# Kernel optimization log

Hardware: AMD Instinct MI355X
Metric: run time of the kernel (lower is better)

The kernel has to match this reference:

```python
import math
import jax, jax.numpy as jnp
import numpy as np

D_MODEL = 1024
NHEAD = 16
DK = D_MODEL // NHEAD
FACTOR = 5
B, L = 4, 8192
U = max(1, min(FACTOR * math.ceil(math.log(L + 1)), L))  # 50


def setup_inputs() -> dict:
    key = jax.random.key(0)
    ks = jax.random.split(key, 10)
    s = 1.0 / math.sqrt(D_MODEL)
    inp = {
        "x": jax.random.normal(ks[0], (B, L, D_MODEL), dtype=jnp.float32),
        "Wq": jax.random.normal(ks[1], (D_MODEL, D_MODEL), dtype=jnp.float32) * s,
        "bq": jnp.zeros((D_MODEL,), dtype=jnp.float32),
        "Wk": jax.random.normal(ks[2], (D_MODEL, D_MODEL), dtype=jnp.float32) * s,
        "bk": jnp.zeros((D_MODEL,), dtype=jnp.float32),
        "Wv": jax.random.normal(ks[3], (D_MODEL, D_MODEL), dtype=jnp.float32) * s,
        "bv": jnp.zeros((D_MODEL,), dtype=jnp.float32),
        "Wo": jax.random.normal(ks[4], (D_MODEL, D_MODEL), dtype=jnp.float32) * s,
        "bo": jnp.zeros((D_MODEL,), dtype=jnp.float32),
        # randperm(L)[:U] sample of key positions (constant, like torch.randperm)
        "idx_k": jax.random.permutation(ks[5], L)[:U].astype(jnp.int32),
    }
    return inp


def reference(x, Wq, bq, Wk, bk, Wv, bv, Wo, bo, idx_k):
    Bv, Lv, _ = x.shape
    H, dk = NHEAD, DK
    u = idx_k.shape[0]
    scale = 1.0 / math.sqrt(dk)

    # projections -> [B, H, L, dk]
    Q = (x @ Wq.T + bq).reshape(Bv, Lv, H, dk).transpose(0, 2, 1, 3)
    K = (x @ Wk.T + bk).reshape(Bv, Lv, H, dk).transpose(0, 2, 1, 3)
    V = (x @ Wv.T + bv).reshape(Bv, Lv, H, dk).transpose(0, 2, 1, 3)

    # sampled scores against u random keys: [B, H, L, u]
    K_samp = K[:, :, idx_k, :]
    scores = jnp.einsum("bhld,bhud->bhlu", Q, K_samp) * scale
    M = scores.max(-1) - scores.mean(-1)                 # [B, H, L]
    _, top_idx = jax.lax.top_k(M, u)                      # [B, H, u]

    # gather selected queries and attend against ALL keys
    Q_top = jnp.take_along_axis(Q, top_idx[..., None], axis=2)   # [B, H, u, dk]
    attn = jax.nn.softmax(jnp.einsum("bhud,bhld->bhul", Q_top, K) * scale, axis=-1)
    ctx_top = jnp.einsum("bhul,bhld->bhud", attn, V)              # [B, H, u, dk]

    # mean(V) fallback, scatter selected contexts back
    ctx = jnp.broadcast_to(V.mean(axis=2, keepdims=True), (Bv, H, Lv, dk))
    bidx = jnp.arange(Bv)[:, None, None]
    hidx = jnp.arange(H)[None, :, None]
    ctx = ctx.at[bidx, hidx, top_idx].set(ctx_top)

    ctx = ctx.transpose(0, 2, 1, 3).reshape(Bv, Lv, H * dk)
    return ctx @ Wo.T + bo
```

## Files before the change

kernel.cpp:

```cpp
#include <hip/hip_runtime.h>
#include <hip/hip_bf16.h>

#define B_ 4
#define L_ 8192
#define D_ 1024
#define H_ 16
#define SCALE 0.125f
#define NC 8
#define QPAD 64
#define RS 72

typedef __attribute__((ext_vector_type(8))) short bf16x8;
typedef __attribute__((ext_vector_type(4))) float f32x4;

__device__ __forceinline__ float blo(unsigned v) { return __uint_as_float(v << 16); }
__device__ __forceinline__ float bhi(unsigned v) { return __uint_as_float(v & 0xffff0000u); }

__device__ __forceinline__ void gl2lds16(const void* g, void* s) {
    __builtin_amdgcn_global_load_lds(
        (const __attribute__((address_space(1))) unsigned int*)g,
        (__attribute__((address_space(3))) unsigned int*)s, 16, 0, 0);
}

__device__ __forceinline__ unsigned short bfbits(float a) {
    __hip_bfloat16 h = __float2bfloat16(a);
    return *(unsigned short*)&h;
}
__device__ __forceinline__ float bf2f(unsigned short u) {
    return __uint_as_float(((unsigned)u) << 16);
}

__global__ __launch_bounds__(256) void split3_kernel(const float* __restrict__ in,
        unsigned short* __restrict__ ph, unsigned short* __restrict__ pm,
        unsigned short* __restrict__ pl, int n4) {
    int i = blockIdx.x * 256 + threadIdx.x;
    if (i >= n4) return;
    float4 v = ((const float4*)in)[i];
    float c[4] = {v.x, v.y, v.z, v.w};
    unsigned short h[4], m[4], l[4];
    #pragma unroll
    for (int j = 0; j < 4; ++j) {
        float a = c[j];
        unsigned short hb = bfbits(a);
        float rh = a - bf2f(hb);
        unsigned short mb = bfbits(rh);
        float rm = rh - bf2f(mb);
        h[j] = hb; m[j] = mb; l[j] = bfbits(rm);
    }
    ((ushort4*)ph)[i] = *(ushort4*)h;
    ((ushort4*)pm)[i] = *(ushort4*)m;
    ((ushort4*)pl)[i] = *(ushort4*)l;
}

__global__ __launch_bounds__(256) void split2_kernel(const float* __restrict__ in,
        unsigned short* __restrict__ ph, unsigned short* __restrict__ pm, int n4) {
    int i = blockIdx.x * 256 + threadIdx.x;
    if (i >= n4) return;
    float4 v = ((const float4*)in)[i];
    float c[4] = {v.x, v.y, v.z, v.w};
    unsigned short h[4], m[4];
    #pragma unroll
    for (int j = 0; j < 4; ++j) {
        float a = c[j];
        unsigned short hb = bfbits(a);
        float rh = a - bf2f(hb);
        h[j] = hb; m[j] = bfbits(rh);
    }
    ((ushort4*)ph)[i] = *(ushort4*)h;
    ((ushort4*)pm)[i] = *(ushort4*)m;
}

__global__ __launch_bounds__(256) void xmean_kernel(const float* __restrict__ x,
                                                    float* __restrict__ xmean) {
    int c = blockIdx.x;
    int j = blockIdx.y * 256 + threadIdx.x;
    int b = blockIdx.z;
    const float* xp = x + ((size_t)b * L_ + (size_t)c * 256) * D_ + j;
    float s = 0.f;
    for (int l = 0; l < 256; ++l) s += xp[(size_t)l * D_];
    atomicAdd(&xmean[b * D_ + j], s * (1.0f / L_));
}

__global__ __launch_bounds__(256) void vecmat_kernel(const float* __restrict__ in,
                                                     const float* __restrict__ W,
                                                     const float* __restrict__ bias,
                                                     float* __restrict__ out) {
    __shared__ float vs[D_];
    int b = blockIdx.y;
    int j = blockIdx.x * 256 + threadIdx.x;
    for (int t = threadIdx.x; t < D_; t += 256) vs[t] = in[b * D_ + t];
    __syncthreads();
    const float* wr = W + (size_t)j * D_;
    float acc = 0.f;
    #pragma unroll 4
    for (int k = 0; k < D_; k += 4) {
        float4 w4 = *(const float4*)(wr + k);
        acc += vs[k] * w4.x + vs[k + 1] * w4.y + vs[k + 2] * w4.z + vs[k + 3] * w4.w;
    }
    out[b * D_ + j] = acc + bias[j];
}

__global__ __launch_bounds__(256) void ksamp_kernel(const float* __restrict__ x,
                                                    const float* __restrict__ Wk,
                                                    const float* __restrict__ bk,
                                                    const int* __restrict__ idx_k,
                                                    float* __restrict__ Ksamp, int U) {
    __shared__ float vs[D_];
    int u = blockIdx.x, b = blockIdx.y;
    int row = idx_k[u];
    const float* xp = x + ((size_t)b * L_ + row) * D_;
    for (int t = threadIdx.x; t < D_; t += 256) vs[t] = xp[t];
    __syncthreads();
    #pragma unroll
    for (int r = 0; r < 4; ++r) {
        int j = r * 256 + threadIdx.x;
        const float* wr = Wk + (size_t)j * D_;
        float acc = 0.f;
        #pragma unroll 4
        for (int k = 0; k < D_; k += 4) {
            float4 w4 = *(const float4*)(wr + k);
            acc += vs[k] * w4.x + vs[k + 1] * w4.y + vs[k + 2] * w4.z + vs[k + 3] * w4.w;
        }
        Ksamp[((size_t)b * U + u) * D_ + j] = acc + bk[j];
    }
}

#define TM 128
#define TN 128
#define BK 32
#define TSZ (TM * BK)

__global__ __launch_bounds__(256) void qkv_mfma(
    const unsigned short* __restrict__ xh, const unsigned short* __restrict__ xm,
    const unsigned short* __restrict__ xl,
    const unsigned short* __restrict__ qh, const unsigned short* __restrict__ qm,
    const unsigned short* __restrict__ ql,
    const unsigned short* __restrict__ kh, const unsigned short* __restrict__ km,
    const unsigned short* __restrict__ vh, const unsigned short* __restrict__ vm,
    const float* __restrict__ bq, const float* __restrict__ bk2, const float* __restrict__ bv,
    float* __restrict__ Q, __hip_bfloat16* __restrict__ Kb, __hip_bfloat16* __restrict__ Vb) {
    __shared__ __align__(16) unsigned short As[3][TSZ];
    __shared__ __align__(16) unsigned short Bs[3][TSZ];

    const int n0 = blockIdx.x * TN;
    const int m0 = blockIdx.y * TM;
    const int tid = threadIdx.x;

    const float* bias; int which; int nb;
    if (n0 < 1024)      { which = 0; nb = n0;        bias = bq;  }
    else if (n0 < 2048) { which = 1; nb = n0 - 1024; bias = bk2; }
    else                { which = 2; nb = n0 - 2048; bias = bv;  }

    const int srow = tid >> 2;
    const int scol = (tid & 3) * 8;

    const int wave = tid >> 6;
    const int lane = tid & 63;
    const int wm = (wave & 1) * 64;
    const int wn = (wave >> 1) * 64;
    const int fr = lane & 15;
    const int fk = (lane >> 4) * 8;
    const int rbase = (lane >> 4) * 4;

    f32x4 acc[4][4];
    #pragma unroll
    for (int i = 0; i < 4; ++i)
        #pragma unroll
        for (int j = 0; j < 4; ++j)
            acc[i][j] = (f32x4){0.f, 0.f, 0.f, 0.f};

    const size_t aBase = (size_t)(m0 + srow) * D_ + scol;
    const size_t bBase = (size_t)(nb + srow) * D_ + scol;

    unsigned short* const As0 = &As[0][0];
    unsigned short* const As1 = &As[1][0];
    unsigned short* const As2 = &As[2][0];
    unsigned short* const Bs0 = &Bs[0][0];
    unsigned short* const Bs1 = &Bs[1][0];
    unsigned short* const Bs2 = &Bs[2][0];

    bf16x8 af[4], bfv[4];
    auto loadA = [&](const unsigned short* t) {
        #pragma unroll
        for (int i = 0; i < 4; ++i)
            af[i] = *(const bf16x8*)(t + (wm + i * 16 + fr) * BK + fk);
    };
    auto loadB = [&](const unsigned short* t) {
        #pragma unroll
        for (int j = 0; j < 4; ++j)
            bfv[j] = *(const bf16x8*)(t + (wn + j * 16 + fr) * BK + fk);
    };
    auto prod = [&]() {
        #pragma unroll
        for (int i = 0; i < 4; ++i)
            #pragma unroll
            for (int j = 0; j < 4; ++j)
                acc[i][j] = __builtin_amdgcn_mfma_f32_16x16x32_bf16(
                    af[i], bfv[j], acc[i][j], 0, 0, 0);
    };
    auto stage = [&](const unsigned short* g, unsigned short* s, int kt, size_t base) {
        gl2lds16(g + base + kt, s + tid * 8);
        gl2lds16(g + base + (size_t)64 * D_ + kt, s + tid * 8 + 2048);
    };

    if (which == 0) {
        for (int kt = 0; kt < D_; kt += BK) {
            stage(xh, As0, kt, aBase);
            stage(xm, As1, kt, aBase);
            stage(xl, As2, kt, aBase);
            stage(qh, Bs0, kt, bBase);
            stage(qm, Bs1, kt, bBase);
            stage(ql, Bs2, kt, bBase);
            __syncthreads();
            loadA(As0); loadB(Bs0); prod();
            loadB(Bs1); prod();
            loadB(Bs2); prod();
            loadA(As1); loadB(Bs0); prod();
            loadB(Bs1); prod();
            loadA(As2); loadB(Bs0); prod();
            __syncthreads();
        }
    } else {
        const unsigned short* Bh = (which == 1) ? kh : vh;
        const unsigned short* Bm = (which == 1) ? km : vm;
        for (int kt = 0; kt < D_; kt += BK) {
            stage(xh, As0, kt, aBase);
            stage(xm, As1, kt, aBase);
            stage(Bh, Bs0, kt, bBase);
            stage(Bm, Bs1, kt, bBase);
            __syncthreads();
            loadA(As0); loadB(Bs0); prod();
            loadB(Bs1); prod();
            loadA(As1); loadB(Bs0); prod();
            __syncthreads();
        }
    }

    float biasv[4];
    #pragma unroll
    for (int j = 0; j < 4; ++j) biasv[j] = bias[nb + wn + j * 16 + fr];

    #pragma unroll
    for (int i = 0; i < 4; ++i) {
        #pragma unroll
        for (int r = 0; r < 4; ++r) {
            size_t row = (size_t)(m0 + wm + i * 16 + rbase + r);
            #pragma unroll
            for (int j = 0; j < 4; ++j) {
                float v = acc[i][j][r] + biasv[j];
                int n = nb + wn + j * 16 + fr;
                if (which == 0)      Q[row * D_ + n] = v;
                else if (which == 1) Kb[row * D_ + n] = __float2bfloat16(v);
                else                 Vb[row * D_ + n] = __float2bfloat16(v);
            }
        }
    }
}

__global__ __launch_bounds__(256) void m_kernel(const float* __restrict__ Q,
                                                const float* __restrict__ Ksamp,
                                                float* __restrict__ M, int U) {
    __shared__ float ks[64 * 64];
    int lc = blockIdx.x, h = blockIdx.y, b = blockIdx.z;
    for (int t = threadIdx.x; t < U * 64; t += 256) {
        int u = t >> 6, d = t & 63;
        ks[t] = Ksamp[((size_t)b * U + u) * D_ + h * 64 + d];
    }
    __syncthreads();
    int l = lc * 256 + threadIdx.x;
    const float* qp = Q + ((size_t)b * L_ + l) * D_ + h * 64;
    float q[64];
    #pragma unroll
    for (int i = 0; i < 16; ++i) *(float4*)&q[i * 4] = *(const float4*)(qp + i * 4);
    float mx = -INFINITY, sm = 0.f;
    for (int u = 0; u < U; ++u) {
        const float* kp = &ks[u * 64];
        float dot = 0.f;
        #pragma unroll
        for (int d = 0; d < 64; ++d) dot = fmaf(q[d], kp[d], dot);
        dot *= SCALE;
        mx = fmaxf(mx, dot);
        sm += dot;
    }
    M[((size_t)(b * H_ + h)) * L_ + l] = mx - sm / (float)U;
}

__global__ __launch_bounds__(256) void topk_kernel(const float* __restrict__ M,
                                                   int* __restrict__ topidx, int U) {
    __shared__ float vals[L_];
    __shared__ float wv[4];
    __shared__ int   wi[4];
    __shared__ int   sbest;
    int bh = blockIdx.x;
    const float* mp = M + (size_t)bh * L_;
    for (int t = threadIdx.x; t < L_; t += 256) vals[t] = mp[t];
    __syncthreads();

    float bv = -INFINITY; int bi = 0x7fffffff;
    for (int t = threadIdx.x; t < L_; t += 256) {
        float v = vals[t];
        if (v > bv || (v == bv && t < bi)) { bv = v; bi = t; }
    }
    const int lane = threadIdx.x & 63, wave = threadIdx.x >> 6;

    for (int u = 0; u < U; ++u) {
        float rv = bv; int ri = bi;
        #pragma unroll
        for (int s = 1; s < 64; s <<= 1) {
            float v2 = __shfl_xor(rv, s, 64);
            int   i2 = __shfl_xor(ri, s, 64);
            if (v2 > rv || (v2 == rv && i2 < ri)) { rv = v2; ri = i2; }
        }
        if (lane == 0) { wv[wave] = rv; wi[wave] = ri; }
        __syncthreads();
        if (threadIdx.x == 0) {
            float fv = wv[0]; int fi = wi[0];
            #pragma unroll
            for (int w = 1; w < 4; ++w) {
                if (wv[w] > fv || (wv[w] == fv && wi[w] < fi)) { fv = wv[w]; fi = wi[w]; }
            }
            topidx[bh * U + u] = fi;
            sbest = fi;
            vals[fi] = -INFINITY;
        }
        __syncthreads();
        int fi = sbest;
        if ((fi & 255) == threadIdx.x) {
            bv = -INFINITY; bi = 0x7fffffff;
            for (int t = threadIdx.x; t < L_; t += 256) {
                float v = vals[t];
                if (v > bv || (v == bv && t < bi)) { bv = v; bi = t; }
            }
        }
    }
}

__global__ __launch_bounds__(256) void attn_mfma(const float* __restrict__ Q,
        const __hip_bfloat16* __restrict__ Kb, const __hip_bfloat16* __restrict__ Vb,
        const int* __restrict__ topidx,
        float* __restrict__ part_m, float* __restrict__ part_s,
        float* __restrict__ part_acc, int U) {
    __shared__ __align__(16) unsigned short Qh[QPAD * RS];
    __shared__ __align__(16) unsigned short Qm[QPAD * RS];
    __shared__ __align__(16) unsigned short Ks[64 * RS];
    __shared__ __align__(16) unsigned short Vt[64 * RS];
    __shared__ __align__(16) unsigned short Ph[QPAD * RS];

    const int c = blockIdx.x, h = blockIdx.y, b = blockIdx.z;
    const int bh = b * H_ + h;
    const int tid = threadIdx.x;
    const int wave = tid >> 6, lane = tid & 63;
    const int w16 = wave * 16;
    const int fr = lane & 15;
    const int quad = lane >> 4;
    const int fk = quad * 8;
    const int l0 = c * (L_ / NC);

    {
        int u = tid >> 2;
        int d0 = (tid & 3) * 16;
        unsigned short hbuf[16], mbuf[16];
        if (u < U) {
            int row = topidx[bh * U + u];
            const float* qp = Q + ((size_t)b * L_ + row) * D_ + h * 64 + d0;
            #pragma unroll
            for (int i = 0; i < 16; ++i) {
                float v = qp[i] * SCALE;
                unsigned short hb = bfbits(v);
                hbuf[i] = hb;
                mbuf[i] = bfbits(v - bf2f(hb));
            }
        } else {
            #pragma unroll
            for (int i = 0; i < 16; ++i) { hbuf[i] = 0; mbuf[i] = 0; }
        }
        #pragma unroll
        for (int i = 0; i < 2; ++i) {
            *(uint4*)&Qh[u * RS + d0 + i * 8] = ((uint4*)hbuf)[i];
            *(uint4*)&Qm[u * RS + d0 + i * 8] = ((uint4*)mbuf)[i];
        }
    }

    float m_r[4], s_r[4];
    f32x4 acc_o[4];
    #pragma unroll
    for (int r = 0; r < 4; ++r) { m_r[r] = -INFINITY; s_r[r] = 0.f; }
    #pragma unroll
    for (int n = 0; n < 4; ++n) acc_o[n] = (f32x4){0.f, 0.f, 0.f, 0.f};

    __syncthreads();

    for (int kt = 0; kt < L_ / NC; kt += 64) {
        {
            int key = tid >> 3;
            int d0 = (tid & 7) * 8;
            const __hip_bfloat16* kp = Kb + ((size_t)b * L_ + l0 + kt) * D_ + h * 64;
            *(uint4*)&Ks[key * RS + d0] = *(const uint4*)(kp + (size_t)key * D_ + d0);
            *(uint4*)&Ks[(key + 32) * RS + d0] =
                *(const uint4*)(kp + (size_t)(key + 32) * D_ + d0);
        }
        {
            int key = tid & 63;
            int g = tid >> 6;
            const __hip_bfloat16* vp = Vb + ((size_t)b * L_ + l0 + kt + key) * D_ + h * 64;
            #pragma unroll
            for (int rr = 0; rr < 2; ++rr) {
                int d0 = rr * 32 + g * 8;
                ushort4 v0 = *(const ushort4*)(vp + d0);
                ushort4 v1 = *(const ushort4*)(vp + d0 + 4);
                Vt[(d0 + 0) * RS + key] = v0.x;
                Vt[(d0 + 1) * RS + key] = v0.y;
                Vt[(d0 + 2) * RS + key] = v0.z;
                Vt[(d0 + 3) * RS + key] = v0.w;
                Vt[(d0 + 4) * RS + key] = v1.x;
                Vt[(d0 + 5) * RS + key] = v1.y;
                Vt[(d0 + 6) * RS + key] = v1.z;
                Vt[(d0 + 7) * RS + key] = v1.w;
            }
        }
        __syncthreads();

        f32x4 sacc[4];
        #pragma unroll
        for (int n = 0; n < 4; ++n) {
            sacc[n] = (f32x4){0.f, 0.f, 0.f, 0.f};
            #pragma unroll
            for (int ks = 0; ks < 2; ++ks) {
                int k0 = ks * 32;
                bf16x8 ah = *(const bf16x8*)&Qh[(w16 + fr) * RS + k0 + fk];
                bf16x8 am = *(const bf16x8*)&Qm[(w16 + fr) * RS + k0 + fk];
                bf16x8 bb = *(const bf16x8*)&Ks[(n * 16 + fr) * RS + k0 + fk];
                sacc[n] = __builtin_amdgcn_mfma_f32_16x16x32_bf16(ah, bb, sacc[n], 0, 0, 0);
                sacc[n] = __builtin_amdgcn_mfma_f32_16x16x32_bf16(am, bb, sacc[n], 0, 0, 0);
            }
        }

        float p[4][4];
        #pragma unroll
        for (int r = 0; r < 4; ++r) {
            float rowmax = fmaxf(fmaxf(sacc[0][r], sacc[1][r]),
                                 fmaxf(sacc[2][r], sacc[3][r]));
            #pragma unroll
            for (int msk = 1; msk <= 8; msk <<= 1)
                rowmax = fmaxf(rowmax, __shfl_xor(rowmax, msk, 64));
            float mnew = fmaxf(m_r[r], rowmax);
            float alpha = __expf(m_r[r] - mnew);
            float rowsum = 0.f;
            #pragma unroll
            for (int n = 0; n < 4; ++n) {
                p[n][r] = __expf(sacc[n][r] - mnew);
                rowsum += p[n][r];
            }
            #pragma unroll
            for (int msk = 1; msk <= 8; msk <<= 1)
                rowsum += __shfl_xor(rowsum, msk, 64);
            s_r[r] = s_r[r] * alpha + rowsum;
            m_r[r] = mnew;
            #pragma unroll
            for (int n = 0; n < 4; ++n) acc_o[n][r] *= alpha;
        }

        #pragma unroll
        for (int r = 0; r < 4; ++r)
            #pragma unroll
            for (int n = 0; n < 4; ++n)
                Ph[(w16 + quad * 4 + r) * RS + n * 16 + fr] = bfbits(p[n][r]);

        #pragma unroll
        for (int n = 0; n < 4; ++n) {
            #pragma unroll
            for (int ks = 0; ks < 2; ++ks) {
                int k0 = ks * 32;
                bf16x8 pa = *(const bf16x8*)&Ph[(w16 + fr) * RS + k0 + fk];
                bf16x8 vb = *(const bf16x8*)&Vt[(n * 16 + fr) * RS + k0 + fk];
                acc_o[n] = __builtin_amdgcn_mfma_f32_16x16x32_bf16(pa, vb, acc_o[n], 0, 0, 0);
            }
        }
        __syncthreads();
    }

    #pragma unroll
    for (int r = 0; r < 4; ++r) {
        int q = w16 + quad * 4 + r;
        if (q < U) {
            size_t base = ((size_t)(bh * QPAD + q)) * NC + c;
            if (fr == 0) { part_m[base] = m_r[r]; part_s[base] = s_r[r]; }
            #pragma unroll
            for (int n = 0; n < 4; ++n)
                part_acc[base * 64 + n * 16 + fr] = acc_o[n][r];
        }
    }
}

__global__ __launch_bounds__(64) void attn_combine(const float* __restrict__ part_m,
        const float* __restrict__ part_s, const float* __restrict__ part_acc,
        float* __restrict__ ctx_top, int U) {
    int u = blockIdx.x, h = blockIdx.y, b = blockIdx.z;
    int bh = b * H_ + h;
    int d = threadIdx.x;
    size_t base = ((size_t)(bh * QPAD + u)) * NC;
    float M = -INFINITY;
    #pragma unroll
    for (int c = 0; c < NC; ++c) M = fmaxf(M, part_m[base + c]);
    float S = 0.f, A = 0.f;
    #pragma unroll
    for (int c = 0; c < NC; ++c) {
        float f = __expf(part_m[base + c] - M);
        S += part_s[base + c] * f;
        A += part_acc[(base + c) * 64 + d] * f;
    }
    ctx_top[(((size_t)bh) * U + u) * 64 + d] = A / S;
}

__global__ __launch_bounds__(256) void fill_base_kernel(const float* __restrict__ base,
                                                        float* __restrict__ out) {
    size_t i = (size_t)blockIdx.x * 256 + threadIdx.x;
    int col4 = (int)(i & 255);
    int b = (int)(i >> 21);
    ((float4*)out)[i] = ((const float4*)base)[b * 256 + col4];
}

__global__ __launch_bounds__(256) void delta_kernel(const float* __restrict__ ctx_top,
        const float* __restrict__ vmean, const float* __restrict__ Wo,
        const int* __restrict__ topidx, float* __restrict__ out, int U) {
    __shared__ float cd[64];
    int u = blockIdx.x, h = blockIdx.y, b = blockIdx.z;
    int row = topidx[(b * H_ + h) * U + u];
    if (threadIdx.x < 64) {
        cd[threadIdx.x] = ctx_top[(((size_t)(b * H_ + h)) * U + u) * 64 + threadIdx.x]
                        - vmean[b * D_ + h * 64 + threadIdx.x];
    }
    __syncthreads();
    float* op = out + ((size_t)b * L_ + row) * D_;
    #pragma unroll
    for (int r = 0; r < 4; ++r) {
        int j = r * 256 + threadIdx.x;
        const float* wr = Wo + (size_t)j * D_ + h * 64;
        float dlt = 0.f;
        #pragma unroll
        for (int k = 0; k < 64; k += 4) {
            float4 w4 = *(const float4*)(wr + k);
            dlt += cd[k] * w4.x + cd[k + 1] * w4.y + cd[k + 2] * w4.z + cd[k + 3] * w4.w;
        }
        atomicAdd(op + j, dlt);
    }
}

extern "C" void kernel_launch(void* const* d_in, const int* in_sizes, int n_in,
                              void* d_out, int out_size, void* d_ws, size_t ws_size,
                              hipStream_t stream) {
    const float* x   = (const float*)d_in[0];
    const float* Wq  = (const float*)d_in[1];
    const float* bq  = (const float*)d_in[2];
    const float* Wk  = (const float*)d_in[3];
    const float* bk  = (const float*)d_in[4];
    const float* Wv  = (const float*)d_in[5];
    const float* bv  = (const float*)d_in[6];
    const float* Wo  = (const float*)d_in[7];
    const float* bo  = (const float*)d_in[8];
    const int* idx_k = (const int*)d_in[9];
    const int U = in_sizes[9];
    float* out = (float*)d_out;
    (void)n_in; (void)ws_size;

    char* ws = (char*)d_ws;
    size_t off = 0;
    auto alloc = [&](size_t bytes) -> void* {
        void* p = ws + off;
        off += (bytes + 255) & ~(size_t)255;
        return p;
    };
    float* Q              = (float*)alloc((size_t)B_ * L_ * D_ * 4);
    __hip_bfloat16* Kb    = (__hip_bfloat16*)alloc((size_t)B_ * L_ * D_ * 2);
    __hip_bfloat16* Vb    = (__hip_bfloat16*)alloc((size_t)B_ * L_ * D_ * 2);
    unsigned short* xh    = (unsigned short*)alloc((size_t)B_ * L_ * D_ * 2);
    unsigned short* xm    = (unsigned short*)alloc((size_t)B_ * L_ * D_ * 2);
    unsigned short* xl    = (unsigned short*)alloc((size_t)B_ * L_ * D_ * 2);
    unsigned short* wqh   = (unsigned short*)alloc((size_t)D_ * D_ * 2);
    unsigned short* wqm   = (unsigned short*)alloc((size_t)D_ * D_ * 2);
    unsigned short* wql   = (unsigned short*)alloc((size_t)D_ * D_ * 2);
    unsigned short* wkh   = (unsigned short*)alloc((size_t)D_ * D_ * 2);
    unsigned short* wkm   = (unsigned short*)alloc((size_t)D_ * D_ * 2);
    unsigned short* wvh   = (unsigned short*)alloc((size_t)D_ * D_ * 2);
    unsigned short* wvm   = (unsigned short*)alloc((size_t)D_ * D_ * 2);
    float* Ksamp          = (float*)alloc((size_t)B_ * 64 * D_ * 4);
    float* Mbuf           = (float*)alloc((size_t)B_ * H_ * L_ * 4);
    int*   topidx         = (int*)alloc((size_t)B_ * H_ * 64 * 4);
    float* xmean          = (float*)alloc((size_t)B_ * D_ * 4);
    float* vmean          = (float*)alloc((size_t)B_ * D_ * 4);
    float* base           = (float*)alloc((size_t)B_ * D_ * 4);
    float* ctxt           = (float*)alloc((size_t)B_ * H_ * 64 * 64 * 4);
    float* part_m         = (float*)alloc((size_t)B_ * H_ * QPAD * NC * 4);
    float* part_s         = (float*)alloc((size_t)B_ * H_ * QPAD * NC * 4);
    float* part_acc       = (float*)alloc((size_t)B_ * H_ * QPAD * NC * 64 * 4);

    hipMemsetAsync(xmean, 0, (size_t)B_ * D_ * 4, stream);
    xmean_kernel<<<dim3(32, 4, B_), 256, 0, stream>>>(x, xmean);
    vecmat_kernel<<<dim3(4, B_), 256, 0, stream>>>(xmean, Wv, bv, vmean);
    vecmat_kernel<<<dim3(4, B_), 256, 0, stream>>>(vmean, Wo, bo, base);
    ksamp_kernel<<<dim3(U, B_), 256, 0, stream>>>(x, Wk, bk, idx_k, Ksamp, U);

    const int n4x = B_ * L_ * D_ / 4;
    const int n4w = D_ * D_ / 4;
    split3_kernel<<<dim3(n4x / 256), 256, 0, stream>>>(x, xh, xm, xl, n4x);
    split3_kernel<<<dim3(n4w / 256), 256, 0, stream>>>(Wq, wqh, wqm, wql, n4w);
    split2_kernel<<<dim3(n4w / 256), 256, 0, stream>>>(Wk, wkh, wkm, n4w);
    split2_kernel<<<dim3(n4w / 256), 256, 0, stream>>>(Wv, wvh, wvm, n4w);

    qkv_mfma<<<dim3(24, 256), 256, 0, stream>>>(xh, xm, xl, wqh, wqm, wql,
                                                wkh, wkm, wvh, wvm,
                                                bq, bk, bv, Q, Kb, Vb);

    m_kernel<<<dim3(32, H_, B_), 256, 0, stream>>>(Q, Ksamp, Mbuf, U);
    topk_kernel<<<dim3(B_ * H_), 256, 0, stream>>>(Mbuf, topidx, U);
    attn_mfma<<<dim3(NC, H_, B_), 256, 0, stream>>>(Q, Kb, Vb, topidx,
                                                    part_m, part_s, part_acc, U);
    attn_combine<<<dim3(U, H_, B_), 64, 0, stream>>>(part_m, part_s, part_acc, ctxt, U);
    fill_base_kernel<<<dim3(out_size / 4 / 256), 256, 0, stream>>>(base, out);
    delta_kernel<<<dim3(U, H_, B_), 256, 0, stream>>>(ctxt, vmean, Wo, topidx, out, U);
}
```

Before: 1.755 ms.

## Split QKV GEMM into fused K/V kernel and Q kernel with swizzled block order

```diff
diff --git a/kernel.cpp b/kernel.cpp
--- a/kernel.cpp
+++ b/kernel.cpp
@@ -12,9 +12,6 @@
 
 typedef __attribute__((ext_vector_type(8))) short bf16x8;
 typedef __attribute__((ext_vector_type(4))) float f32x4;
-
-__device__ __forceinline__ float blo(unsigned v) { return __uint_as_float(v << 16); }
-__device__ __forceinline__ float bhi(unsigned v) { return __uint_as_float(v & 0xffff0000u); }
 
 __device__ __forceinline__ void gl2lds16(const void* g, void* s) {
     __builtin_amdgcn_global_load_lds(
@@ -130,26 +127,20 @@
 #define BK 32
 #define TSZ (TM * BK)
 
-__global__ __launch_bounds__(256) void qkv_mfma(
+__global__ __launch_bounds__(256) void qkv_mfma_q(
     const unsigned short* __restrict__ xh, const unsigned short* __restrict__ xm,
     const unsigned short* __restrict__ xl,
     const unsigned short* __restrict__ qh, const unsigned short* __restrict__ qm,
     const unsigned short* __restrict__ ql,
-    const unsigned short* __restrict__ kh, const unsigned short* __restrict__ km,
-    const unsigned short* __restrict__ vh, const unsigned short* __restrict__ vm,
-    const float* __restrict__ bq, const float* __restrict__ bk2, const float* __restrict__ bv,
-    float* __restrict__ Q, __hip_bfloat16* __restrict__ Kb, __hip_bfloat16* __restrict__ Vb) {
+    const float* __restrict__ bq, float* __restrict__ Q) {
     __shared__ __align__(16) unsigned short As[3][TSZ];
     __shared__ __align__(16) unsigned short Bs[3][TSZ];
 
-    const int n0 = blockIdx.x * TN;
-    const int m0 = blockIdx.y * TM;
+    const int f  = blockIdx.y * 8 + blockIdx.x;
+    const int w  = (f & 7) * 256 + (f >> 3);
+    const int n0 = (w & 7) * TN;
+    const int m0 = (w >> 3) * TM;
     const int tid = threadIdx.x;
-
-    const float* bias; int which; int nb;
-    if (n0 < 1024)      { which = 0; nb = n0;        bias = bq;  }
-    else if (n0 < 2048) { which = 1; nb = n0 - 1024; bias = bk2; }
-    else                { which = 2; nb = n0 - 2048; bias = bv;  }
 
     const int srow = tid >> 2;
     const int scol = (tid & 3) * 8;
@@ -170,14 +161,7 @@
             acc[i][j] = (f32x4){0.f, 0.f, 0.f, 0.f};
 
     const size_t aBase = (size_t)(m0 + srow) * D_ + scol;
-    const size_t bBase = (size_t)(nb + srow) * D_ + scol;
-
-    unsigned short* const As0 = &As[0][0];
-    unsigned short* const As1 = &As[1][0];
-    unsigned short* const As2 = &As[2][0];
-    unsigned short* const Bs0 = &Bs[0][0];
-    unsigned short* const Bs1 = &Bs[1][0];
-    unsigned short* const Bs2 = &Bs[2][0];
+    const size_t bBase = (size_t)(n0 + srow) * D_ + scol;
 
     bf16x8 af[4], bfv[4];
     auto loadA = [&](const unsigned short* t) {
@@ -203,42 +187,26 @@
         gl2lds16(g + base + (size_t)64 * D_ + kt, s + tid * 8 + 2048);
     };
 
-    if (which == 0) {
-        for (int kt = 0; kt < D_; kt += BK) {
-            stage(xh, As0, kt, aBase);
-            stage(xm, As1, kt, aBase);
-            stage(xl, As2, kt, aBase);
-            stage(qh, Bs0, kt, bBase);
-            stage(qm, Bs1, kt, bBase);
-            stage(ql, Bs2, kt, bBase);
-            __syncthreads();
-            loadA(As0); loadB(Bs0); prod();
-            loadB(Bs1); prod();
-            loadB(Bs2); prod();
-            loadA(As1); loadB(Bs0); prod();
-            loadB(Bs1); prod();
-            loadA(As2); loadB(Bs0); prod();
-            __syncthreads();
-        }
-    } else {
-        const unsigned short* Bh = (which == 1) ? kh : vh;
-        const unsigned short* Bm = (which == 1) ? km : vm;
-        for (int kt = 0; kt < D_; kt += BK) {
-            stage(xh, As0, kt, aBase);
-            stage(xm, As1, kt, aBase);
-            stage(Bh, Bs0, kt, bBase);
-            stage(Bm, Bs1, kt, bBase);
-            __syncthreads();
-            loadA(As0); loadB(Bs0); prod();
-            loadB(Bs1); prod();
-            loadA(As1); loadB(Bs0); prod();
-            __syncthreads();
-        }
+    for (int kt = 0; kt < D_; kt += BK) {
+        stage(xh, &As[0][0], kt, aBase);
+        stage(xm, &As[1][0], kt, aBase);
+        stage(xl, &As[2][0], kt, aBase);
+        stage(qh, &Bs[0][0], kt, bBase);
+        stage(qm, &Bs[1][0], kt, bBase);
+        stage(ql, &Bs[2][0], kt, bBase);
+        __syncthreads();
+        loadA(&As[0][0]); loadB(&Bs[0][0]); prod();
+        loadB(&Bs[1][0]); prod();
+        loadB(&Bs[2][0]); prod();
+        loadA(&As[1][0]); loadB(&Bs[0][0]); prod();
+        loadB(&Bs[1][0]); prod();
+        loadA(&As[2][0]); loadB(&Bs[0][0]); prod();
+        __syncthreads();
     }
 
     float biasv[4];
     #pragma unroll
-    for (int j = 0; j < 4; ++j) biasv[j] = bias[nb + wn + j * 16 + fr];
+    for (int j = 0; j < 4; ++j) biasv[j] = bq[n0 + wn + j * 16 + fr];
 
     #pragma unroll
     for (int i = 0; i < 4; ++i) {
@@ -247,11 +215,119 @@
             size_t row = (size_t)(m0 + wm + i * 16 + rbase + r);
             #pragma unroll
             for (int j = 0; j < 4; ++j) {
-                float v = acc[i][j][r] + biasv[j];
-                int n = nb + wn + j * 16 + fr;
-                if (which == 0)      Q[row * D_ + n] = v;
-                else if (which == 1) Kb[row * D_ + n] = __float2bfloat16(v);
-                else                 Vb[row * D_ + n] = __float2bfloat16(v);
+                int n = n0 + wn + j * 16 + fr;
+                Q[row * D_ + n] = acc[i][j][r] + biasv[j];
+            }
+        }
+    }
+}
+
+__global__ __launch_bounds__(256) void qkv_mfma_kv(
+    const unsigned short* __restrict__ xh, const unsigned short* __restrict__ xm,
+    const unsigned short* __restrict__ kh, const unsigned short* __restrict__ km,
+    const unsigned short* __restrict__ vh, const unsigned short* __restrict__ vm,
+    const float* __restrict__ bk2, const float* __restrict__ bv,
+    __hip_bfloat16* __restrict__ Kb, __hip_bfloat16* __restrict__ Vb) {
+    __shared__ __align__(16) unsigned short As[2][TSZ];
+    __shared__ __align__(16) unsigned short Bs[4][TSZ];
+
+    const int f  = blockIdx.y * 8 + blockIdx.x;
+    const int w  = (f & 7) * 256 + (f >> 3);
+    const int n0 = (w & 7) * TN;
+    const int m0 = (w >> 3) * TM;
+    const int tid = threadIdx.x;
+
+    const int srow = tid >> 2;
+    const int scol = (tid & 3) * 8;
+
+    const int wave = tid >> 6;
+    const int lane = tid & 63;
+    const int wm = (wave & 1) * 64;
+    const int wn = (wave >> 1) * 64;
+    const int fr = lane & 15;
+    const int fk = (lane >> 4) * 8;
+    const int rbase = (lane >> 4) * 4;
+
+    f32x4 accK[4][4], accV[4][4];
+    #pragma unroll
+    for (int i = 0; i < 4; ++i)
+        #pragma unroll
+        for (int j = 0; j < 4; ++j) {
+            accK[i][j] = (f32x4){0.f, 0.f, 0.f, 0.f};
+            accV[i][j] = (f32x4){0.f, 0.f, 0.f, 0.f};
+        }
+
+    const size_t aBase = (size_t)(m0 + srow) * D_ + scol;
+    const size_t bBase = (size_t)(n0 + srow) * D_ + scol;
+
+    bf16x8 af[4], bfv[4];
+    auto loadA = [&](const unsigned short* t) {
+        #pragma unroll
+        for (int i = 0; i < 4; ++i)
+            af[i] = *(const bf16x8*)(t + (wm + i * 16 + fr) * BK + fk);
+    };
+    auto loadB = [&](const unsigned short* t) {
+        #pragma unroll
+        for (int j = 0; j < 4; ++j)
+            bfv[j] = *(const bf16x8*)(t + (wn + j * 16 + fr) * BK + fk);
+    };
+    auto prodK = [&]() {
+        #pragma unroll
+        for (int i = 0; i < 4; ++i)
+            #pragma unroll
+            for (int j = 0; j < 4; ++j)
+                accK[i][j] = __builtin_amdgcn_mfma_f32_16x16x32_bf16(
+                    af[i], bfv[j], accK[i][j], 0, 0, 0);
+    };
+    auto prodV = [&]() {
+        #pragma unroll
+        for (int i = 0; i < 4; ++i)
+            #pragma unroll
+            for (int j = 0; j < 4; ++j)
+                accV[i][j] = __builtin_amdgcn_mfma_f32_16x16x32_bf16(
+                    af[i], bfv[j], accV[i][j], 0, 0, 0);
+    };
+    auto stage = [&](const unsigned short* g, unsigned short* s, int kt, size_t base) {
+        gl2lds16(g + base + kt, s + tid * 8);
+        gl2lds16(g + base + (size_t)64 * D_ + kt, s + tid * 8 + 2048);
+    };
+
+    for (int kt = 0; kt < D_; kt += BK) {
+        stage(xh, &As[0][0], kt, aBase);
+        stage(xm, &As[1][0], kt, aBase);
+        stage(kh, &Bs[0][0], kt, bBase);
+        stage(km, &Bs[1][0], kt, bBase);
+        stage(vh, &Bs[2][0], kt, bBase);
+        stage(vm, &Bs[3][0], kt, bBase);
+        __syncthreads();
+        loadA(&As[0][0]);
+        loadB(&Bs[0][0]); prodK();
+        loadB(&Bs[1][0]); prodK();
+        loadB(&Bs[2][0]); prodV();
+        loadB(&Bs[3][0]); prodV();
+        loadA(&As[1][0]);
+        loadB(&Bs[0][0]); prodK();
+        loadB(&Bs[2][0]); prodV();
+        __syncthreads();
+    }
+
+    float biasK[4], biasV[4];
+    #pragma unroll
+    for (int j = 0; j < 4; ++j) {
+        biasK[j] = bk2[n0 + wn + j * 16 + fr];
+        biasV[j] = bv[n0 + wn + j * 16 + fr];
+    }
+
+    #pragma unroll
+    for (int i = 0; i < 4; ++i) {
+        #pragma unroll
+        for (int r = 0; r < 4; ++r) {
+            size_t row = (size_t)(m0 + wm + i * 16 + rbase + r);
+            #pragma unroll
+            for (int j = 0; j < 4; ++j) {
+                int n = n0 + wn + j * 16 + fr;
+                Kb[row * D_ + n] = __float2bfloat16(accK[i][j][r] + biasK[j]);
+                Vb[row * D_ + n] = __float2bfloat16(accV[i][j][r] + biasV[j]);
             }
         }
     }
@@ -400,23 +476,15 @@
                 *(const uint4*)(kp + (size_t)(key + 32) * D_ + d0);
         }
         {
-            int key = tid & 63;
-            int g = tid >> 6;
-            const __hip_bfloat16* vp = Vb + ((size_t)b * L_ + l0 + kt + key) * D_ + h * 64;
-            #pragma unroll
-            for (int rr = 0; rr < 2; ++rr) {
-                int d0 = rr * 32 + g * 8;
-                ushort4 v0 = *(const ushort4*)(vp + d0);
-                ushort4 v1 = *(const ushort4*)(vp + d0 + 4);
-                Vt[(d0 + 0) * RS + key] = v0.x;
-                Vt[(d0 + 1) * RS + key] = v0.y;
-                Vt[(d0 + 2) * RS + key] = v0.z;
-                Vt[(d0 + 3) * RS + key] = v0.w;
-                Vt[(d0 + 4) * RS + key] = v1.x;
-                Vt[(d0 + 5) * RS + key] = v1.y;
-                Vt[(d0 + 6) * RS + key] = v1.z;
-                Vt[(d0 + 7) * RS + key] = v1.w;
-            }
+            int key = tid >> 2;
+            int d0 = (tid & 3) * 16;
+            const __hip_bfloat16* vp =
+                Vb + ((size_t)b * L_ + l0 + kt + key) * D_ + h * 64 + d0;
+            unsigned short vbuf[16];
+            *(uint4*)&vbuf[0] = *(const uint4*)(vp);
+            *(uint4*)&vbuf[8] = *(const uint4*)(vp + 8);
+            #pragma unroll
+            for (int i = 0; i < 16; ++i) Vt[(d0 + i) * RS + key] = vbuf[i];
         }
         __syncthreads();
 
@@ -605,11 +673,12 @@
     split3_kernel<<<dim3(n4x / 256), 256, 0, stream>>>(x, xh, xm, xl, n4x);
     split3_kernel<<<dim3(n4w / 256), 256, 0, stream>>>(Wq, wqh, wqm, wql, n4w);
     split2_kernel<<<dim3(n4w / 256), 256, 0, stream>>>(Wk, wkh, wkm, n4w);
-    split2_kernel<<<dim3(n4w / 256), 256, 0, stream>>>(Wv, wvh, wvm, n4w);
-
-    qkv_mfma<<<dim3(24, 256), 256, 0, stream>>>(xh, xm, xl, wqh, wqm, wql,
-                                                wkh, wkm, wvh, wvm,
-                                                bq, bk, bv, Q, Kb, Vb);
+    split2_kernel<<<dim3(n4w / 256), 256, 0, stream>>>(Wv, wvm ? wvh : wvh, wvm, n4w);
+
+    qkv_mfma_kv<<<dim3(8, 256), 256, 0, stream>>>(xh, xm, wkh, wkm, wvh, wvm,
+                                                  bk, bv, Kb, Vb);
+    qkv_mfma_q<<<dim3(8, 256), 256, 0, stream>>>(xh, xm, xl, wqh, wqm, wql,
+                                                 bq, Q);
 
     m_kernel<<<dim3(32, H_, B_), 256, 0, stream>>>(Q, Ksamp, Mbuf, U);
     topk_kernel<<<dim3(B_ * H_), 256, 0, stream>>>(Mbuf, topidx, U);
```

Result: slower. 1.867 ms (+6.4%).
